# Kernel tuning notes

Hardware: AMD Instinct MI355X
Metric: run time of the kernel (lower is better)

The kernel has to match this reference:

```python
import jax, jax.numpy as jnp
import numpy as np

T, D, I, E, K = 2048, 2048, 5632, 8, 2


def setup_inputs() -> dict:
    key = jax.random.key(0)
    k1, k2, k3, k4, k5 = jax.random.split(key, 5)
    s = 0.02
    return {
        "x": jax.random.normal(k1, (T, D), dtype=jnp.float32),
        "gate_w": jax.random.normal(k2, (E, D), dtype=jnp.float32) * s,
        "w_gate": jax.random.normal(k3, (E, I, D), dtype=jnp.float32) * s,
        "w_up": jax.random.normal(k4, (E, I, D), dtype=jnp.float32) * s,
        "w_down": jax.random.normal(k5, (E, D, I), dtype=jnp.float32) * s,
    }


def reference(x, gate_w, w_gate, w_up, w_down):
    # Router: logits [T, E], top-k then softmax over the k selected logits
    logits = x @ gate_w.T
    top_vals, top_idx = jax.lax.top_k(logits, K)          # [T, K]
    rw = jax.nn.softmax(top_vals, axis=-1)                # [T, K]
    # Dense combine weights [T, E]: sum of routing weights over selected slots.
    # Mathematically identical to the per-(expert, slot) scatter-add in torch,
    # since duplicate selections of the same expert just sum their weights.
    combine = jnp.sum(jax.nn.one_hot(top_idx, E, dtype=x.dtype) * rw[..., None], axis=1)  # [T, E]
    # SwiGLU expert MLPs, batched over experts (grouped GEMM as dense einsum)
    g = jnp.einsum("td,eid->tei", x, w_gate)              # [T, E, I]
    u = jnp.einsum("td,eid->tei", x, w_up)                # [T, E, I]
    h = jax.nn.silu(g) * u                                 # [T, E, I]
    out_e = jnp.einsum("tei,edi->ted", h, w_down)         # [T, E, D]
    return jnp.einsum("ted,te->td", out_e, combine)       # [T, D]
```

## Files before the change

kernel.cpp:

```cpp
#include <hip/hip_runtime.h>
#include <hip/hip_bf16.h>
#include <stdint.h>

#define TTOK 2048
#define DDIM 2048
#define IDIM 5632
#define NEXP 8

typedef __attribute__((ext_vector_type(8))) short bf16x8;
typedef __attribute__((ext_vector_type(4))) float f32x4;
typedef __attribute__((ext_vector_type(8))) unsigned short u16x8;
typedef __attribute__((ext_vector_type(4))) unsigned short u16x4;

__device__ __forceinline__ unsigned short f2bf(float f) {
  union { float f; uint32_t u; } v; v.f = f;
  uint32_t u = v.u + 0x7fffu + ((v.u >> 16) & 1u);
  return (unsigned short)(u >> 16);
}

__device__ __forceinline__ uint32_t fbits(float f) {
  union { float f; uint32_t u; } v; v.f = f; return v.u;
}

__device__ __forceinline__ u16x8 cvt8t(float4 a, float4 b) {
  union { u16x8 v; uint32_t w[4]; } r;
  r.w[0] = __builtin_amdgcn_perm(fbits(a.y), fbits(a.x), 0x07060302);
  r.w[1] = __builtin_amdgcn_perm(fbits(a.w), fbits(a.z), 0x07060302);
  r.w[2] = __builtin_amdgcn_perm(fbits(b.y), fbits(b.x), 0x07060302);
  r.w[3] = __builtin_amdgcn_perm(fbits(b.w), fbits(b.z), 0x07060302);
  return r.v;
}

typedef __attribute__((address_space(3))) void lds_t;
typedef const __attribute__((address_space(1))) void gbl_t;
__device__ __forceinline__ void gload16(const void* g, void* l) {
  __builtin_amdgcn_global_load_lds((gbl_t*)g, (lds_t*)l, 16, 0, 0);
}

#define PIPE_BAR1() asm volatile("s_waitcnt vmcnt(20) lgkmcnt(0)\n\ts_barrier" ::: "memory")
#define PIPE_BAR2() asm volatile("s_barrier" ::: "memory")

__global__ __launch_bounds__(256) void router_kernel(
    const float* __restrict__ x, const float* __restrict__ gw,
    unsigned short* __restrict__ xbf,
    int* __restrict__ cnt, int* __restrict__ slots, float* __restrict__ wts)
{
  const int lane = threadIdx.x & 63;
  const int t = (blockIdx.x * blockDim.x + threadIdx.x) >> 6;
  const float* xr = x + (size_t)t * DDIM;
  float acc[NEXP];
#pragma unroll
  for (int e = 0; e < NEXP; ++e) acc[e] = 0.f;
#pragma unroll
  for (int it = 0; it < DDIM / 256; ++it) {
    const int d = (it * 64 + lane) * 4;
    const float4 xv = *(const float4*)(xr + d);
    u16x4 xb; xb[0]=f2bf(xv.x); xb[1]=f2bf(xv.y); xb[2]=f2bf(xv.z); xb[3]=f2bf(xv.w);
    *(u16x4*)(xbf + (size_t)t * DDIM + d) = xb;
#pragma unroll
    for (int e = 0; e < NEXP; ++e) {
      const float4 gv = *(const float4*)(gw + (size_t)e * DDIM + d);
      acc[e] += xv.x*gv.x + xv.y*gv.y + xv.z*gv.z + xv.w*gv.w;
    }
  }
#pragma unroll
  for (int e = 0; e < NEXP; ++e) {
    float v = acc[e];
#pragma unroll
    for (int off = 32; off > 0; off >>= 1) v += __shfl_xor(v, off);
    acc[e] = v;
  }
  if (lane == 0) {
    int i0 = 0; float v0 = acc[0];
#pragma unroll
    for (int e = 1; e < NEXP; ++e) if (acc[e] > v0) { v0 = acc[e]; i0 = e; }
    int i1 = -1; float v1 = -3.4e38f;
#pragma unroll
    for (int e = 0; e < NEXP; ++e) { if (e == i0) continue; if (acc[e] > v1) { v1 = acc[e]; i1 = e; } }
    const float e1 = __expf(v1 - v0);
    const float w0 = 1.f / (1.f + e1);
    const float w1 = e1 / (1.f + e1);
    const int p0 = atomicAdd(&cnt[i0], 1);
    slots[i0 * TTOK + p0] = t * 2;     wts[i0 * TTOK + p0] = w0;
    const int p1 = atomicAdd(&cnt[i1], 1);
    slots[i1 * TTOK + p1] = t * 2 + 1; wts[i1 * TTOK + p1] = w1;
  }
}

__global__ void plan_kernel(const int* __restrict__ cnt,
                            int* __restrict__ tilemap, int* __restrict__ ntiles)
{
  if (threadIdx.x == 0 && blockIdx.x == 0) {
    int n = 0;
#pragma unroll
    for (int e = 0; e < NEXP; ++e) {
      const int nt = (cnt[e] + 127) >> 7;
      for (int m = 0; m < nt; ++m) tilemap[n++] = (e << 8) | m;
    }
    ntiles[0] = n;
  }
}


__global__ __launch_bounds__(256) void gateup_kernel(
    const unsigned short* __restrict__ xbf,
    const float* __restrict__ wg, const float* __restrict__ wu,
    const int* __restrict__ cnt, const int* __restrict__ slots,
    const int* __restrict__ tilemap, const int* __restrict__ ntiles,
    unsigned short* __restrict__ h)
{
  const int flat = (blockIdx.x & 7) * 440 + (blockIdx.x >> 3);
  const int ti = flat % 40;
  if (ti >= ntiles[0]) return;
  const int em = tilemap[ti];
  const int e = em >> 8;
  const int mt = em & 255;
  const int n0 = (flat / 40) * 64;
  const int count = cnt[e];
  const int m0 = mt * 128;

  __shared__ unsigned short A[2][128][64];
  __shared__ unsigned short Bg[64][64];
  __shared__ unsigned short Bu[64][64];
  __shared__ int rslot[128];
  __shared__ int rtok[128];

  const int tid = threadIdx.x;
  const int lane = tid & 63;
  const int wid = tid >> 6;

  if (tid < 128) {
    const int idx = m0 + tid;
    const int safe = slots[e * TTOK + m0];
    const int s = (idx < count) ? slots[e * TTOK + idx] : safe;
    rslot[tid] = (idx < count) ? s : -1;
    rtok[tid] = s >> 1;
  }
  __syncthreads();

  const int aswz = ((lane & 7) ^ ((lane >> 3) & 7)) * 8;
  const unsigned short* aptr[4];
#pragma unroll
  for (int j = 0; j < 4; ++j) {
    const int arow = wid * 32 + j * 8 + (lane >> 3);
    aptr[j] = xbf + (size_t)rtok[arow] * DDIM + aswz;
  }

  const int brow = tid >> 2;
  const int bcb = (tid & 3) * 2;
  const int bswz = brow & 7;
  const size_t wboff = (size_t)e * IDIM * DDIM + (size_t)(n0 + brow) * DDIM + bcb * 8;
  const float* gsrc = wg + wboff;
  const float* usrc = wu + wboff;

  const int wr = wid >> 1, wc = wid & 1;
  const int fr = lane & 15;
  const int kc = lane >> 4;
  const int rsw = fr & 7;

  f32x4 accg[4][2] = {};
  f32x4 accu[4][2] = {};

  float4 Pg[2][4], Pu[2][4];
#pragma unroll
  for (int j = 0; j < 4; ++j) gload16(aptr[j], &A[0][wid * 32][0] + j * 512);
#pragma unroll
  for (int q = 0; q < 4; ++q) { Pg[0][q] = *(const float4*)(gsrc + q * 4);      Pu[0][q] = *(const float4*)(usrc + q * 4); }
#pragma unroll
  for (int q = 0; q < 4; ++q) { Pg[1][q] = *(const float4*)(gsrc + 64 + q * 4); Pu[1][q] = *(const float4*)(usrc + 64 + q * 4); }

#pragma unroll 2
  for (int t = 0; t < 32; ++t) {
    const int cur = t & 1;
    const int st = t & 1;
    const int kp  = (t < 31) ? (t + 1) * 64 : 31 * 64;
    const int kp2 = (t + 2 <= 31) ? (t + 2) * 64 : 31 * 64;

#pragma unroll
    for (int j = 0; j < 4; ++j) gload16(aptr[j] + kp, &A[cur ^ 1][wid * 32][0] + j * 512);
    __builtin_amdgcn_sched_barrier(0);
#pragma unroll
    for (int qq = 0; qq < 2; ++qq) {
      const int oc = ((bcb + qq) ^ bswz) * 8;
      *(u16x8*)&Bg[brow][oc] = cvt8t(Pg[st][qq * 2], Pg[st][qq * 2 + 1]);
      *(u16x8*)&Bu[brow][oc] = cvt8t(Pu[st][qq * 2], Pu[st][qq * 2 + 1]);
    }
#pragma unroll
    for (int q = 0; q < 4; ++q) { Pg[st][q] = *(const float4*)(gsrc + kp2 + q * 4); Pu[st][q] = *(const float4*)(usrc + kp2 + q * 4); }
    PIPE_BAR1();

    __builtin_amdgcn_s_setprio(1);
#pragma unroll
    for (int kk = 0; kk < 2; ++kk) {
      bf16x8 a[4], bg[2], bu[2];
      const int cs = ((kk * 4 + kc) ^ rsw) * 8;
#pragma unroll
      for (int mf = 0; mf < 4; ++mf)
        a[mf] = *(const bf16x8*)&A[cur][wr * 64 + mf * 16 + fr][cs];
#pragma unroll
      for (int nf = 0; nf < 2; ++nf) {
        bg[nf] = *(const bf16x8*)&Bg[wc * 32 + nf * 16 + fr][cs];
        bu[nf] = *(const bf16x8*)&Bu[wc * 32 + nf * 16 + fr][cs];
      }
#pragma unroll
      for (int mf = 0; mf < 4; ++mf)
#pragma unroll
        for (int nf = 0; nf < 2; ++nf) {
          accg[mf][nf] = __builtin_amdgcn_mfma_f32_16x16x32_bf16(a[mf], bg[nf], accg[mf][nf], 0, 0, 0);
          accu[mf][nf] = __builtin_amdgcn_mfma_f32_16x16x32_bf16(a[mf], bu[nf], accu[mf][nf], 0, 0, 0);
        }
    }
    __builtin_amdgcn_s_setprio(0);

    PIPE_BAR2();
  }

#pragma unroll
  for (int mf = 0; mf < 4; ++mf)
#pragma unroll
    for (int nf = 0; nf < 2; ++nf)
#pragma unroll
      for (int j = 0; j < 4; ++j) {
        const int r = wr * 64 + mf * 16 + (lane >> 4) * 4 + j;
        const int s = rslot[r];
        if (s >= 0) {
          const float g = accg[mf][nf][j];
          const float u = accu[mf][nf][j];
          const float hv = g / (1.f + __expf(-g)) * u;
          h[(size_t)s * IDIM + n0 + wc * 32 + nf * 16 + fr] = f2bf(hv);
        }
      }
}

__global__ __launch_bounds__(256) void down_kernel(
    const unsigned short* __restrict__ h,
    const float* __restrict__ wd,
    const int* __restrict__ cnt, const int* __restrict__ slots,
    const float* __restrict__ wts,
    const int* __restrict__ tilemap, const int* __restrict__ ntiles,
    float* __restrict__ out)
{
  const int flat = (blockIdx.x & 7) * 160 + (blockIdx.x >> 3);
  const int ti = flat % 40;
  if (ti >= ntiles[0]) return;
  const int em = tilemap[ti];
  const int e = em >> 8;
  const int mt = em & 255;
  const int r2 = flat / 40;
  const int n0 = (r2 & 15) * 128;
  const int ks = r2 >> 4;
  const int kbase = ks * (IDIM / 2);
  const int count = cnt[e];
  const int m0 = mt * 128;

  __shared__ unsigned short A[2][128][64];
  __shared__ unsigned short B[128][64];
  __shared__ int rslot[128];
  __shared__ float rw[128];

  const int tid = threadIdx.x;
  const int lane = tid & 63;
  const int wid = tid >> 6;

  if (tid < 128) {
    const int idx = m0 + tid;
    const int safe = slots[e * TTOK + m0];
    const int s = (idx < count) ? slots[e * TTOK + idx] : safe;
    rslot[tid] = (idx < count) ? s : (safe | 0x40000000);
    rw[tid] = (idx < count) ? wts[e * TTOK + idx] : 0.f;
  }
  __syncthreads();

  const int aswz = ((lane & 7) ^ ((lane >> 3) & 7)) * 8;
  const unsigned short* aptr[4];
#pragma unroll
  for (int j = 0; j < 4; ++j) {
    const int arow = wid * 32 + j * 8 + (lane >> 3);
    aptr[j] = h + (size_t)(rslot[arow] & 0x3fffffff) * IDIM + kbase + aswz;
  }

  const int brow = tid >> 1;
  const int bcb = (tid & 1) * 4;
  const int bswz = brow & 7;
  const float* bsrc = wd + (size_t)e * DDIM * IDIM + (size_t)(n0 + brow) * IDIM + kbase + bcb * 8;

  const int wr = wid >> 1, wc = wid & 1;
  const int fr = lane & 15;
  const int kc = lane >> 4;
  const int rsw = fr & 7;

  f32x4 acc[4][4] = {};

  float4 Pb[2][8];
#pragma unroll
  for (int j = 0; j < 4; ++j) gload16(aptr[j], &A[0][wid * 32][0] + j * 512);
#pragma unroll
  for (int q = 0; q < 8; ++q) Pb[0][q] = *(const float4*)(bsrc + q * 4);
#pragma unroll
  for (int q = 0; q < 8; ++q) Pb[1][q] = *(const float4*)(bsrc + 64 + q * 4);

#pragma unroll 2
  for (int t = 0; t < 44; ++t) {
    const int cur = t & 1;
    const int st = t & 1;
    const int kp  = (t < 43) ? (t + 1) * 64 : 43 * 64;
    const int kp2 = (t + 2 <= 43) ? (t + 2) * 64 : 43 * 64;

#pragma unroll
    for (int j = 0; j < 4; ++j) gload16(aptr[j] + kp, &A[cur ^ 1][wid * 32][0] + j * 512);
    __builtin_amdgcn_sched_barrier(0);
#pragma unroll
    for (int qq = 0; qq < 4; ++qq)
      *(u16x8*)&B[brow][((bcb + qq) ^ bswz) * 8] = cvt8t(Pb[st][qq * 2], Pb[st][qq * 2 + 1]);
#pragma unroll
    for (int q = 0; q < 8; ++q) Pb[st][q] = *(const float4*)(bsrc + kp2 + q * 4);
    PIPE_BAR1();

    __builtin_amdgcn_s_setprio(1);
#pragma unroll
    for (int kk = 0; kk < 2; ++kk) {
      bf16x8 a[4], b[4];
      const int cs = ((kk * 4 + kc) ^ rsw) * 8;
#pragma unroll
      for (int mf = 0; mf < 4; ++mf)
        a[mf] = *(const bf16x8*)&A[cur][wr * 64 + mf * 16 + fr][cs];
#pragma unroll
      for (int nf = 0; nf < 4; ++nf)
        b[nf] = *(const bf16x8*)&B[wc * 64 + nf * 16 + fr][cs];
#pragma unroll
      for (int mf = 0; mf < 4; ++mf)
#pragma unroll
        for (int nf = 0; nf < 4; ++nf)
          acc[mf][nf] = __builtin_amdgcn_mfma_f32_16x16x32_bf16(a[mf], b[nf], acc[mf][nf], 0, 0, 0);
    }
    __builtin_amdgcn_s_setprio(0);

    PIPE_BAR2();
  }

#pragma unroll
  for (int mf = 0; mf < 4; ++mf)
#pragma unroll
    for (int j = 0; j < 4; ++j) {
      const int r = wr * 64 + mf * 16 + (lane >> 4) * 4 + j;
      const int s = rslot[r];
      if (!(s & 0x40000000)) {
        const int t2 = s >> 1;
        const float w = rw[r];
#pragma unroll
        for (int nf = 0; nf < 4; ++nf)
          atomicAdd(out + (size_t)t2 * DDIM + n0 + wc * 64 + nf * 16 + fr,
                    acc[mf][nf][j] * w);
      }
    }
}

extern "C" void kernel_launch(void* const* d_in, const int* in_sizes, int n_in,
                              void* d_out, int out_size, void* d_ws, size_t ws_size,
                              hipStream_t stream) {
  const float* x  = (const float*)d_in[0];
  const float* gw = (const float*)d_in[1];
  const float* wg = (const float*)d_in[2];
  const float* wu = (const float*)d_in[3];
  const float* wd = (const float*)d_in[4];
  float* out = (float*)d_out;

  char* ws = (char*)d_ws;
  unsigned short* xbf = (unsigned short*)ws;
  unsigned short* h   = (unsigned short*)(ws + 8388608);
  int*   slots = (int*)(ws + 8388608 + 46137344);
  float* wts   = (float*)(ws + 8388608 + 46137344 + 65536);
  int*   cnt   = (int*)(ws + 8388608 + 46137344 + 131072);
  int*   tmap  = (int*)(ws + 8388608 + 46137344 + 131072 + 32);
  int*   ntl   = (int*)(ws + 8388608 + 46137344 + 131072 + 288);

  hipMemsetAsync(cnt, 0, NEXP * sizeof(int), stream);
  hipMemsetAsync(d_out, 0, (size_t)TTOK * DDIM * sizeof(float), stream);

  router_kernel<<<TTOK / 4, 256, 0, stream>>>(x, gw, xbf, cnt, slots, wts);
  plan_kernel<<<1, 64, 0, stream>>>(cnt, tmap, ntl);
  gateup_kernel<<<3520, 256, 0, stream>>>(xbf, wg, wu, cnt, slots, tmap, ntl, h);
  down_kernel<<<1280, 256, 0, stream>>>(h, wd, cnt, slots, wts, tmap, ntl, out);
}
```

Baseline: 874.2 us.

## Double-buffer weight tiles in LDS and use one barrier per k-step

Both grouped GEMM kernels now keep the converted bf16 weight tile in two LDS buffers. The next tile is written to the alternate buffer while the MFMAs read the current one. The register staging drops from two prefetch stages to one, and the two barriers per iteration collapse into one wait-plus-barrier at the end of the step. This removes a synchronization point and lets the LDS stores overlap compute, at the cost of more LDS per block, which may lower occupancy, and a shallower global-load prefetch distance.

```diff
diff --git a/kernel.cpp b/kernel.cpp
--- a/kernel.cpp
+++ b/kernel.cpp
@@ -37,8 +37,7 @@
   __builtin_amdgcn_global_load_lds((gbl_t*)g, (lds_t*)l, 16, 0, 0);
 }
 
-#define PIPE_BAR1() asm volatile("s_waitcnt vmcnt(20) lgkmcnt(0)\n\ts_barrier" ::: "memory")
-#define PIPE_BAR2() asm volatile("s_barrier" ::: "memory")
+#define PIPE_WAIT_BAR() asm volatile("s_waitcnt vmcnt(8) lgkmcnt(0)\n\ts_barrier" ::: "memory")
 
 __global__ __launch_bounds__(256) void router_kernel(
     const float* __restrict__ x, const float* __restrict__ gw,
@@ -120,8 +119,8 @@
   const int m0 = mt * 128;
 
   __shared__ unsigned short A[2][128][64];
-  __shared__ unsigned short Bg[64][64];
-  __shared__ unsigned short Bu[64][64];
+  __shared__ unsigned short Bg[2][64][64];
+  __shared__ unsigned short Bu[2][64][64];
   __shared__ int rslot[128];
   __shared__ int rtok[128];
 
@@ -161,19 +160,25 @@
   f32x4 accg[4][2] = {};
   f32x4 accu[4][2] = {};
 
-  float4 Pg[2][4], Pu[2][4];
+  float4 Pg[4], Pu[4];
 #pragma unroll
   for (int j = 0; j < 4; ++j) gload16(aptr[j], &A[0][wid * 32][0] + j * 512);
 #pragma unroll
-  for (int q = 0; q < 4; ++q) { Pg[0][q] = *(const float4*)(gsrc + q * 4);      Pu[0][q] = *(const float4*)(usrc + q * 4); }
-#pragma unroll
-  for (int q = 0; q < 4; ++q) { Pg[1][q] = *(const float4*)(gsrc + 64 + q * 4); Pu[1][q] = *(const float4*)(usrc + 64 + q * 4); }
+  for (int q = 0; q < 4; ++q) { Pg[q] = *(const float4*)(gsrc + q * 4); Pu[q] = *(const float4*)(usrc + q * 4); }
+#pragma unroll
+  for (int qq = 0; qq < 2; ++qq) {
+    const int oc = ((bcb + qq) ^ bswz) * 8;
+    *(u16x8*)&Bg[0][brow][oc] = cvt8t(Pg[qq * 2], Pg[qq * 2 + 1]);
+    *(u16x8*)&Bu[0][brow][oc] = cvt8t(Pu[qq * 2], Pu[qq * 2 + 1]);
+  }
+#pragma unroll
+  for (int q = 0; q < 4; ++q) { Pg[q] = *(const float4*)(gsrc + 64 + q * 4); Pu[q] = *(const float4*)(usrc + 64 + q * 4); }
+  PIPE_WAIT_BAR();
 
 #pragma unroll 2
   for (int t = 0; t < 32; ++t) {
     const int cur = t & 1;
-    const int st = t & 1;
-    const int kp  = (t < 31) ? (t + 1) * 64 : 31 * 64;
+    const int kp  = (t + 1 <= 31) ? (t + 1) * 64 : 31 * 64;
     const int kp2 = (t + 2 <= 31) ? (t + 2) * 64 : 31 * 64;
 
 #pragma unroll
@@ -182,12 +187,12 @@
 #pragma unroll
     for (int qq = 0; qq < 2; ++qq) {
       const int oc = ((bcb + qq) ^ bswz) * 8;
-      *(u16x8*)&Bg[brow][oc] = cvt8t(Pg[st][qq * 2], Pg[st][qq * 2 + 1]);
-      *(u16x8*)&Bu[brow][oc] = cvt8t(Pu[st][qq * 2], Pu[st][qq * 2 + 1]);
-    }
-#pragma unroll
-    for (int q = 0; q < 4; ++q) { Pg[st][q] = *(const float4*)(gsrc + kp2 + q * 4); Pu[st][q] = *(const float4*)(usrc + kp2 + q * 4); }
-    PIPE_BAR1();
+      *(u16x8*)&Bg[cur ^ 1][brow][oc] = cvt8t(Pg[qq * 2], Pg[qq * 2 + 1]);
+      *(u16x8*)&Bu[cur ^ 1][brow][oc] = cvt8t(Pu[qq * 2], Pu[qq * 2 + 1]);
+    }
+#pragma unroll
+    for (int q = 0; q < 4; ++q) { Pg[q] = *(const float4*)(gsrc + kp2 + q * 4); Pu[q] = *(const float4*)(usrc + kp2 + q * 4); }
+    __builtin_amdgcn_sched_barrier(0);
 
     __builtin_amdgcn_s_setprio(1);
 #pragma unroll
@@ -199,8 +204,8 @@
         a[mf] = *(const bf16x8*)&A[cur][wr * 64 + mf * 16 + fr][cs];
 #pragma unroll
       for (int nf = 0; nf < 2; ++nf) {
-        bg[nf] = *(const bf16x8*)&Bg[wc * 32 + nf * 16 + fr][cs];
-        bu[nf] = *(const bf16x8*)&Bu[wc * 32 + nf * 16 + fr][cs];
+        bg[nf] = *(const bf16x8*)&Bg[cur][wc * 32 + nf * 16 + fr][cs];
+        bu[nf] = *(const bf16x8*)&Bu[cur][wc * 32 + nf * 16 + fr][cs];
       }
 #pragma unroll
       for (int mf = 0; mf < 4; ++mf)
@@ -212,7 +217,7 @@
     }
     __builtin_amdgcn_s_setprio(0);
 
-    PIPE_BAR2();
+    PIPE_WAIT_BAR();
   }
 
 #pragma unroll
@@ -254,7 +259,7 @@
   const int m0 = mt * 128;
 
   __shared__ unsigned short A[2][128][64];
-  __shared__ unsigned short B[128][64];
+  __shared__ unsigned short B[2][128][64];
   __shared__ int rslot[128];
   __shared__ float rw[128];
 
@@ -291,19 +296,22 @@
 
   f32x4 acc[4][4] = {};
 
-  float4 Pb[2][8];
+  float4 Pb[8];
 #pragma unroll
   for (int j = 0; j < 4; ++j) gload16(aptr[j], &A[0][wid * 32][0] + j * 512);
 #pragma unroll
-  for (int q = 0; q < 8; ++q) Pb[0][q] = *(const float4*)(bsrc + q * 4);
-#pragma unroll
-  for (int q = 0; q < 8; ++q) Pb[1][q] = *(const float4*)(bsrc + 64 + q * 4);
+  for (int q = 0; q < 8; ++q) Pb[q] = *(const float4*)(bsrc + q * 4);
+#pragma unroll
+  for (int qq = 0; qq < 4; ++qq)
+    *(u16x8*)&B[0][brow][((bcb + qq) ^ bswz) * 8] = cvt8t(Pb[qq * 2], Pb[qq * 2 + 1]);
+#pragma unroll
+  for (int q = 0; q < 8; ++q) Pb[q] = *(const float4*)(bsrc + 64 + q * 4);
+  PIPE_WAIT_BAR();
 
 #pragma unroll 2
   for (int t = 0; t < 44; ++t) {
     const int cur = t & 1;
-    const int st = t & 1;
-    const int kp  = (t < 43) ? (t + 1) * 64 : 43 * 64;
+    const int kp  = (t + 1 <= 43) ? (t + 1) * 64 : 43 * 64;
     const int kp2 = (t + 2 <= 43) ? (t + 2) * 64 : 43 * 64;
 
 #pragma unroll
@@ -311,10 +319,10 @@
     __builtin_amdgcn_sched_barrier(0);
 #pragma unroll
     for (int qq = 0; qq < 4; ++qq)
-      *(u16x8*)&B[brow][((bcb + qq) ^ bswz) * 8] = cvt8t(Pb[st][qq * 2], Pb[st][qq * 2 + 1]);
-#pragma unroll
-    for (int q = 0; q < 8; ++q) Pb[st][q] = *(const float4*)(bsrc + kp2 + q * 4);
-    PIPE_BAR1();
+      *(u16x8*)&B[cur ^ 1][brow][((bcb + qq) ^ bswz) * 8] = cvt8t(Pb[qq * 2], Pb[qq * 2 + 1]);
+#pragma unroll
+    for (int q = 0; q < 8; ++q) Pb[q] = *(const float4*)(bsrc + kp2 + q * 4);
+    __builtin_amdgcn_sched_barrier(0);
 
     __builtin_amdgcn_s_setprio(1);
 #pragma unroll
@@ -326,7 +334,7 @@
         a[mf] = *(const bf16x8*)&A[cur][wr * 64 + mf * 16 + fr][cs];
 #pragma unroll
       for (int nf = 0; nf < 4; ++nf)
-        b[nf] = *(const bf16x8*)&B[wc * 64 + nf * 16 + fr][cs];
+        b[nf] = *(const bf16x8*)&B[cur][wc * 64 + nf * 16 + fr][cs];
 #pragma unroll
       for (int mf = 0; mf < 4; ++mf)
 #pragma unroll
@@ -335,7 +343,7 @@
     }
     __builtin_amdgcn_s_setprio(0);
 
-    PIPE_BAR2();
+    PIPE_WAIT_BAR();
   }
 
 #pragma unroll
```

Result: no change. 858.2 us (-1.8%).
